# Kernel tuning notes

Hardware: AMD Instinct MI355X
Metric: run time of the kernel (lower is better)

The kernel has to match this reference:

```python
import jax, jax.numpy as jnp
import numpy as np

N_NODES = 50000
N_EDGES = 800000
F = 128
LN_EPS = 1e-5


def _sage_conv(h, src, dst, Wl, bl, Wr, n_nodes):
    # PyG SAGEConv (aggr='mean', root_weight=True):
    #   out_i = lin_l(mean_{j->i} h_j) + lin_r(h_i)
    msg = h[src]  # [E, F] irregular gather
    s = jax.ops.segment_sum(msg, dst, num_segments=n_nodes)  # [N, F]
    deg = jax.ops.segment_sum(jnp.ones((src.shape[0],), h.dtype), dst,
                              num_segments=n_nodes)  # [N]
    mean = s / jnp.maximum(deg, 1.0)[:, None]
    return mean @ Wl.T + bl + h @ Wr.T


def _graph_layernorm(h, w, b):
    # PyG LayerNorm mode='graph', batch=None: normalize over ALL entries,
    # eps added to std, then per-channel affine.
    m = h.mean()
    std = jnp.sqrt(jnp.mean((h - m) ** 2))
    return (h - m) / (std + LN_EPS) * w + b


def _prelu(h, w):
    # nn.PReLU(1): single shared slope
    return jnp.where(h >= 0, h, w * h)


def setup_inputs() -> dict:
    key = jax.random.key(0)
    ks = jax.random.split(key, 12)
    sc = 1.0 / np.sqrt(F)
    x = jax.random.normal(ks[0], (N_NODES, F), dtype=jnp.float32)
    edge_index = jax.random.randint(ks[1], (2, N_EDGES), 0, N_NODES, dtype=jnp.int64)
    return {
        "x": x,
        "edge_index": edge_index,
        "Wl0": jax.random.uniform(ks[2], (F, F), jnp.float32, -sc, sc),
        "bl0": jnp.zeros((F,), jnp.float32),
        "Wr0": jax.random.uniform(ks[3], (F, F), jnp.float32, -sc, sc),
        "ln_w0": jnp.ones((F,), jnp.float32),
        "ln_b0": jnp.zeros((F,), jnp.float32),
        "pw0": jnp.full((1,), 0.25, jnp.float32),
        "skipW0": jax.random.uniform(ks[4], (F, F), jnp.float32, -sc, sc),
        "Wl1": jax.random.uniform(ks[5], (F, F), jnp.float32, -sc, sc),
        "bl1": jnp.zeros((F,), jnp.float32),
        "Wr1": jax.random.uniform(ks[6], (F, F), jnp.float32, -sc, sc),
        "ln_w1": jnp.ones((F,), jnp.float32),
        "ln_b1": jnp.zeros((F,), jnp.float32),
        "pw1": jnp.full((1,), 0.25, jnp.float32),
    }


def reference(x, edge_index, Wl0, bl0, Wr0, ln_w0, ln_b0, pw0, skipW0,
              Wl1, bl1, Wr1, ln_w1, ln_b1, pw1):
    src, dst = edge_index[0], edge_index[1]
    n = x.shape[0]
    # layer 0: h = x
    h = _sage_conv(x, src, dst, Wl0, bl0, Wr0, n)
    h = _graph_layernorm(h, ln_w0, ln_b0)
    h1 = _prelu(h, pw0)
    # layer 1: h = skip(x) + h1
    h = x @ skipW0.T + h1
    h = _sage_conv(h, src, dst, Wl1, bl1, Wr1, n)
    h = _graph_layernorm(h, ln_w1, ln_b1)
    h = _prelu(h, pw1)
    return h
```

## Files before the change

kernel.cpp:

```cpp
#include <hip/hip_runtime.h>

#define LN_EPS 1e-5f
#define BUCKCAP 2048
#define PCHUNK 6656
#define PK 13

typedef short bf16x8 __attribute__((ext_vector_type(8)));
typedef float f32x4  __attribute__((ext_vector_type(4)));

static __device__ __forceinline__ float4 ld4(const float* p){ return *(const float4*)p; }
static __device__ __forceinline__ uint f2bf1(float f){
  uint u = __float_as_uint(f);
  return (u + 0x7fffu + ((u >> 16) & 1u)) >> 16;
}
static __device__ __forceinline__ float bf2f(uint lo16){ return __uint_as_float(lo16 << 16); }

__global__ void detect_fmt_kernel(const int* __restrict__ ei, int* __restrict__ flag,
                                  double* __restrict__ stats, int* __restrict__ bcnt){
  __shared__ int any;
  if (threadIdx.x == 0) any = 0;
  __syncthreads();
  int nz = 0;
  for (int i = threadIdx.x; i < 1024; i += 256)
    nz |= (ei[2*i+1] != 0);
  if (nz) atomicOr(&any, 1);
  for (int i = threadIdx.x; i < 1024; i += 256) bcnt[i] = 0;
  if (threadIdx.x < 4) stats[threadIdx.x] = 0.0;
  __syncthreads();
  if (threadIdx.x == 0) *flag = any;
}

__global__ __launch_bounds__(512) void partition_kernel(
    const int* __restrict__ ei, int E, const int* __restrict__ flag,
    int* __restrict__ bucket_count, uint* __restrict__ ebuf){
  __shared__ int hist[1024];
  __shared__ int base[1024];
  __shared__ int cur[1024];
  const int tid = threadIdx.x;
  const int lo = blockIdx.x * PCHUNK;
  const int hi = min(lo + PCHUNK, E);
  hist[tid] = 0; hist[tid + 512] = 0;
  __syncthreads();

  const int fmt = *flag;
  uint pd[PK];
  #pragma unroll
  for (int k = 0; k < PK; k++){
    int e = lo + tid + k*512;
    uint v = 0xffffffffu;
    if (e < hi){
      int s, d;
      if (fmt){ s = ei[e]; d = ei[E + e]; }
      else    { s = ei[2*e]; d = ei[2*(E + e)]; }
      v = ((uint)d << 16) | (uint)s;
      atomicAdd(&hist[v >> 22], 1);
    }
    pd[k] = v;
  }
  __syncthreads();
  #pragma unroll
  for (int t0 = 0; t0 < 2; t0++){
    int t = tid + t0*512;
    int h = hist[t];
    base[t] = (h > 0) ? atomicAdd(&bucket_count[t], h) : 0;
    cur[t] = 0;
  }
  __syncthreads();
  #pragma unroll
  for (int k = 0; k < PK; k++){
    int e = lo + tid + k*512;
    if (e < hi){
      uint v = pd[k];
      int b = v >> 22;
      int pos = base[b] + atomicAdd(&cur[b], 1);
      if (pos < BUCKCAP) ebuf[(size_t)b*BUCKCAP + pos] = v;
    }
  }
}

__global__ void convert_bf16_kernel(const float* __restrict__ src, ushort* __restrict__ dst, int n8){
  int i = blockIdx.x*256 + threadIdx.x;
  if (i >= n8) return;
  float4 a = ld4(src + (size_t)i*8);
  float4 b = ld4(src + (size_t)i*8 + 4);
  uint4 o;
  o.x = f2bf1(a.x) | (f2bf1(a.y) << 16);
  o.y = f2bf1(a.z) | (f2bf1(a.w) << 16);
  o.z = f2bf1(b.x) | (f2bf1(b.y) << 16);
  o.w = f2bf1(b.z) | (f2bf1(b.w) << 16);
  *(uint4*)(dst + (size_t)i*8) = o;
}

__global__ void convert_w_kernel(const float* __restrict__ s0, const float* __restrict__ s1,
                                 const float* __restrict__ s2, const float* __restrict__ s3,
                                 const float* __restrict__ s4, ushort* __restrict__ dst){
  int i = blockIdx.x*256 + threadIdx.x;
  if (i >= 10240) return;
  int m = i >> 11;
  int o = (i & 2047) * 8;
  const float* s = (m == 0) ? s0 : (m == 1) ? s1 : (m == 2) ? s2 : (m == 3) ? s3 : s4;
  float4 a = ld4(s + o);
  float4 b = ld4(s + o + 4);
  uint4 v;
  v.x = f2bf1(a.x) | (f2bf1(a.y) << 16);
  v.y = f2bf1(a.z) | (f2bf1(a.w) << 16);
  v.z = f2bf1(b.x) | (f2bf1(b.y) << 16);
  v.w = f2bf1(b.z) | (f2bf1(b.w) << 16);
  *(uint4*)(dst + (size_t)m*16384 + o) = v;
}

__global__ __launch_bounds__(512) void bucket_aggregate(const ushort* __restrict__ h,
    const uint* __restrict__ ebuf, const int* __restrict__ bucket_count,
    ushort* __restrict__ outmean, int N){
  __shared__ ushort ssrc[BUCKCAP];
  __shared__ int lcnt[64], lofs[64], lcur[64];
  const int tid = threadIdx.x;
  const int b = blockIdx.x;
  const int n0 = b << 6;
  const uint* eb = ebuf + (size_t)b*BUCKCAP;
  const int cnt = min(bucket_count[b], BUCKCAP);

  if (tid < 64) lcnt[tid] = 0;
  __syncthreads();
  for (int e = tid; e < cnt; e += 512)
    atomicAdd(&lcnt[(eb[e] >> 16) & 63], 1);
  __syncthreads();
  if (tid < 64){
    int v = lcnt[tid];
    int s = v;
    #pragma unroll
    for (int off = 1; off < 64; off <<= 1){
      int u = __shfl_up(s, off);
      if (tid >= off) s += u;
    }
    lofs[tid] = s - v;
    lcur[tid] = s - v;
  }
  __syncthreads();
  for (int e = tid; e < cnt; e += 512){
    uint v = eb[e];
    int pos = atomicAdd(&lcur[(v >> 16) & 63], 1);
    ssrc[pos] = (ushort)(v & 0xffffu);
  }
  __syncthreads();

  const int wv = tid >> 6, lane = tid & 63;
  const uint* hp = (const uint*)h;
  uint* op = (uint*)outmean;
  #pragma unroll 1
  for (int i = 0; i < 8; i++){
    int j = wv*8 + i;
    int node = n0 + j;
    if (node >= N) break;
    int start = lofs[j];
    int d = lcnt[j];
    float ax = 0.f, ay = 0.f;
    int e = 0;
    for (; e + 8 <= d; e += 8){
      uint v0 = hp[(size_t)ssrc[start+e+0]*64 + lane];
      uint v1 = hp[(size_t)ssrc[start+e+1]*64 + lane];
      uint v2 = hp[(size_t)ssrc[start+e+2]*64 + lane];
      uint v3 = hp[(size_t)ssrc[start+e+3]*64 + lane];
      uint v4 = hp[(size_t)ssrc[start+e+4]*64 + lane];
      uint v5 = hp[(size_t)ssrc[start+e+5]*64 + lane];
      uint v6 = hp[(size_t)ssrc[start+e+6]*64 + lane];
      uint v7 = hp[(size_t)ssrc[start+e+7]*64 + lane];
      ax += bf2f(v0 & 0xffffu) + bf2f(v1 & 0xffffu) + bf2f(v2 & 0xffffu) + bf2f(v3 & 0xffffu)
          + bf2f(v4 & 0xffffu) + bf2f(v5 & 0xffffu) + bf2f(v6 & 0xffffu) + bf2f(v7 & 0xffffu);
      ay += bf2f(v0 >> 16) + bf2f(v1 >> 16) + bf2f(v2 >> 16) + bf2f(v3 >> 16)
          + bf2f(v4 >> 16) + bf2f(v5 >> 16) + bf2f(v6 >> 16) + bf2f(v7 >> 16);
    }
    for (; e < d; e++){
      uint v = hp[(size_t)ssrc[start+e]*64 + lane];
      ax += bf2f(v & 0xffffu);
      ay += bf2f(v >> 16);
    }
    float inv = 1.f / fmaxf((float)d, 1.f);
    op[(size_t)node*64 + lane] = f2bf1(ax*inv) | (f2bf1(ay*inv) << 16);
  }
}

__global__ __launch_bounds__(256) void gemm_dual_mfma(
    const ushort* __restrict__ A1, const ushort* __restrict__ A2,
    const ushort* __restrict__ W1, const ushort* __restrict__ W2,
    const float* __restrict__ bias, float* __restrict__ out,
    int N, double* __restrict__ stats){
  const int tid  = threadIdx.x;
  const int lane = tid & 63;
  const int wv   = tid >> 6;
  const int r0   = blockIdx.x*128 + wv*32;
  const int lrow = lane & 15;
  const int lk   = (lane >> 4) * 8;

  f32x4 acc[2][8] = {};

  #pragma unroll
  for (int ks = 0; ks < 4; ks++){
    const int kb = ks*32 + lk;
    bf16x8 a1[2], a2[2];
    #pragma unroll
    for (int m = 0; m < 2; m++){
      int r = r0 + m*16 + lrow;
      if (r > N-1) r = N-1;
      a1[m] = *(const bf16x8*)(A1 + (size_t)r*128 + kb);
      a2[m] = *(const bf16x8*)(A2 + (size_t)r*128 + kb);
    }
    #pragma unroll
    for (int n = 0; n < 8; n++){
      const int c = n*16 + lrow;
      bf16x8 b1 = *(const bf16x8*)(W1 + c*128 + kb);
      bf16x8 b2 = *(const bf16x8*)(W2 + c*128 + kb);
      #pragma unroll
      for (int m = 0; m < 2; m++){
        acc[m][n] = __builtin_amdgcn_mfma_f32_16x16x32_bf16(a1[m], b1, acc[m][n], 0, 0, 0);
        acc[m][n] = __builtin_amdgcn_mfma_f32_16x16x32_bf16(a2[m], b2, acc[m][n], 0, 0, 0);
      }
    }
  }

  float bn[8];
  #pragma unroll
  for (int n = 0; n < 8; n++) bn[n] = bias[n*16 + lrow];

  double ls1 = 0.0, ls2 = 0.0;
  const int rb = (lane >> 4) * 4;
  #pragma unroll
  for (int m = 0; m < 2; m++){
    #pragma unroll
    for (int j = 0; j < 4; j++){
      int r = r0 + m*16 + rb + j;
      if (r < N){
        #pragma unroll
        for (int n = 0; n < 8; n++){
          float v = acc[m][n][j] + bn[n];
          out[(size_t)r*128 + n*16 + lrow] = v;
          ls1 += (double)v;
          ls2 += (double)v * (double)v;
        }
      }
    }
  }
  #pragma unroll
  for (int off = 32; off > 0; off >>= 1){
    ls1 += __shfl_down(ls1, off);
    ls2 += __shfl_down(ls2, off);
  }
  __shared__ double red[8];
  if (lane == 0){ red[wv*2] = ls1; red[wv*2+1] = ls2; }
  __syncthreads();
  if (tid == 0) atomicAdd(&stats[0], red[0]+red[2]+red[4]+red[6]);
  if (tid == 1) atomicAdd(&stats[1], red[1]+red[3]+red[5]+red[7]);
}

__global__ __launch_bounds__(256) void gemm_skip_mfma(
    const ushort* __restrict__ A, const ushort* __restrict__ W,
    const float* __restrict__ T0, const double* __restrict__ stats,
    const float* __restrict__ lnw, const float* __restrict__ lnb,
    const float* __restrict__ pw,
    ushort* __restrict__ outb, int N, double inv_cnt){
  const int tid  = threadIdx.x;
  const int lane = tid & 63;
  const int wv   = tid >> 6;
  const int r0   = blockIdx.x*128 + wv*32;
  const int lrow = lane & 15;
  const int lk   = (lane >> 4) * 8;

  f32x4 acc[2][8] = {};

  #pragma unroll
  for (int ks = 0; ks < 4; ks++){
    const int kb = ks*32 + lk;
    bf16x8 a[2];
    #pragma unroll
    for (int m = 0; m < 2; m++){
      int r = r0 + m*16 + lrow;
      if (r > N-1) r = N-1;
      a[m] = *(const bf16x8*)(A + (size_t)r*128 + kb);
    }
    #pragma unroll
    for (int n = 0; n < 8; n++){
      const int c = n*16 + lrow;
      bf16x8 b = *(const bf16x8*)(W + c*128 + kb);
      #pragma unroll
      for (int m = 0; m < 2; m++)
        acc[m][n] = __builtin_amdgcn_mfma_f32_16x16x32_bf16(a[m], b, acc[m][n], 0, 0, 0);
    }
  }

  double s1 = stats[0], s2 = stats[1];
  double md = s1 * inv_cnt;
  double var = s2 * inv_cnt - md*md;
  float mean = (float)md;
  float rstd = 1.f / ((float)sqrt(fmax(var, 0.0)) + LN_EPS);
  float slope = pw[0];
  float wn[8], bb[8];
  #pragma unroll
  for (int n = 0; n < 8; n++){
    wn[n] = lnw[n*16 + lrow];
    bb[n] = lnb[n*16 + lrow];
  }

  const int rb = (lane >> 4) * 4;
  #pragma unroll
  for (int m = 0; m < 2; m++){
    #pragma unroll
    for (int j = 0; j < 4; j++){
      int r = r0 + m*16 + rb + j;
      if (r < N){
        #pragma unroll
        for (int n = 0; n < 8; n++){
          float t = T0[(size_t)r*128 + n*16 + lrow];
          float l = (t - mean)*rstd*wn[n] + bb[n];
          l = (l >= 0.f) ? l : slope*l;
          float v = acc[m][n][j] + l;
          outb[(size_t)r*128 + n*16 + lrow] = (ushort)f2bf1(v);
        }
      }
    }
  }
}

__global__ __launch_bounds__(256) void ln_prelu_kernel(
    const float* __restrict__ T, const double* __restrict__ stats,
    const float* __restrict__ lnw, const float* __restrict__ lnb,
    const float* __restrict__ pw, float* __restrict__ out,
    int nf4, double inv_cnt){
  double s1 = stats[0], s2 = stats[1];
  double md = s1 * inv_cnt;
  double var = s2 * inv_cnt - md*md;
  float mean = (float)md;
  float rstd = 1.f / ((float)sqrt(fmax(var, 0.0)) + LN_EPS);
  float slope = pw[0];
  for (int i = blockIdx.x*256 + threadIdx.x; i < nf4; i += gridDim.x*256){
    int c4 = i & 31;
    float4 t = ld4(T + (size_t)i*4);
    float4 w4 = ld4(lnw + c4*4);
    float4 b4 = ld4(lnb + c4*4);
    float4 v; float l;
    l = (t.x - mean)*rstd*w4.x + b4.x; v.x = (l >= 0.f ? l : slope*l);
    l = (t.y - mean)*rstd*w4.y + b4.y; v.y = (l >= 0.f ? l : slope*l);
    l = (t.z - mean)*rstd*w4.z + b4.z; v.z = (l >= 0.f ? l : slope*l);
    l = (t.w - mean)*rstd*w4.w + b4.w; v.w = (l >= 0.f ? l : slope*l);
    *(float4*)(out + (size_t)i*4) = v;
  }
}

extern "C" void kernel_launch(void* const* d_in, const int* in_sizes, int n_in,
                              void* d_out, int out_size, void* d_ws, size_t ws_size,
                              hipStream_t stream){
  const float* x    = (const float*)d_in[0];
  const int*   ei   = (const int*)d_in[1];
  const float* Wl0  = (const float*)d_in[2];
  const float* bl0  = (const float*)d_in[3];
  const float* Wr0  = (const float*)d_in[4];
  const float* lnw0 = (const float*)d_in[5];
  const float* lnb0 = (const float*)d_in[6];
  const float* pw0  = (const float*)d_in[7];
  const float* skW  = (const float*)d_in[8];
  const float* Wl1  = (const float*)d_in[9];
  const float* bl1  = (const float*)d_in[10];
  const float* Wr1  = (const float*)d_in[11];
  const float* lnw1 = (const float*)d_in[12];
  const float* lnb1 = (const float*)d_in[13];
  const float* pw1  = (const float*)d_in[14];

  const int N = in_sizes[0] / 128;
  const int E = in_sizes[1] / 2;

  char* p = (char*)d_ws;
  auto carve = [&](size_t bytes)->char*{
    char* r = p;
    p += (bytes + 255) & ~(size_t)255;
    return r;
  };
  double* stats   = (double*)carve(4*sizeof(double));
  int*    flag    = (int*)carve(sizeof(int));
  int*    bcnt    = (int*)carve((size_t)1024*4);
  uint*   ebuf    = (uint*)carve((size_t)1024*BUCKCAP*4);
  ushort* x16     = (ushort*)carve((size_t)N*128*2);
  ushort* mean16  = (ushort*)carve((size_t)N*128*2);
  ushort* hskip16 = (ushort*)carve((size_t)N*128*2);
  ushort* wbuf    = (ushort*)carve((size_t)5*16384*2);
  float*  tbuf    = (float*)d_out;

  ushort* Wl0_16 = wbuf;
  ushort* Wr0_16 = wbuf + 16384;
  ushort* skW_16 = wbuf + 32768;
  ushort* Wl1_16 = wbuf + 49152;
  ushort* Wr1_16 = wbuf + 65536;

  const int nbuck = (N + 63) >> 6;
  const int pb = (E + PCHUNK - 1) / PCHUNK;
  detect_fmt_kernel<<<1, 256, 0, stream>>>(ei, flag, stats, bcnt);
  partition_kernel<<<pb, 512, 0, stream>>>(ei, E, flag, bcnt, ebuf);
  convert_bf16_kernel<<<(N*16 + 255)/256, 256, 0, stream>>>(x, x16, N*16);
  convert_w_kernel<<<40, 256, 0, stream>>>(Wl0, Wr0, skW, Wl1, Wr1, wbuf);

  int gb = (N + 127)/128;
  double inv_cnt = 1.0 / ((double)N * 128.0);

  bucket_aggregate<<<nbuck, 512, 0, stream>>>(x16, ebuf, bcnt, mean16, N);
  gemm_dual_mfma<<<gb, 256, 0, stream>>>(mean16, x16, Wl0_16, Wr0_16, bl0, tbuf, N, stats);
  gemm_skip_mfma<<<gb, 256, 0, stream>>>(x16, skW_16, tbuf, stats, lnw0, lnb0, pw0, hskip16, N, inv_cnt);
  bucket_aggregate<<<nbuck, 512, 0, stream>>>(hskip16, ebuf, bcnt, mean16, N);
  gemm_dual_mfma<<<gb, 256, 0, stream>>>(mean16, hskip16, Wl1_16, Wr1_16, bl1, tbuf, N, stats + 2);
  ln_prelu_kernel<<<2048, 256, 0, stream>>>(tbuf, stats + 2, lnw1, lnb1, pw1, (float*)d_out, N*32, inv_cnt);
}
```

Before: 269.6 us.

## Fuse GEMM, graph layernorm and PReLU via software grid barrier; merge prep kernels

Each layer's dual GEMM now keeps its accumulators in registers, reduces global stats, waits on an atomic-counter grid barrier, then applies layernorm, PReLU and (layer 0) the skip GEMM in place. This removes the fp32 intermediate round trip through global memory and the separate skip and layernorm kernels. Format detection moves into the partition kernel, and the x/weight conversions plus counter zeroing are merged into one prep kernel, cutting launches. The grid barrier needs all 391 blocks to be co-resident, which launch_bounds(256,2) is meant to allow; if they are not, it deadlocks.

Measured after the change: 312.0 us. 1.16x slower.

```diff
diff --git a/kernel.cpp b/kernel.cpp
--- a/kernel.cpp
+++ b/kernel.cpp
@@ -15,34 +15,63 @@
 }
 static __device__ __forceinline__ float bf2f(uint lo16){ return __uint_as_float(lo16 << 16); }
 
-__global__ void detect_fmt_kernel(const int* __restrict__ ei, int* __restrict__ flag,
-                                  double* __restrict__ stats, int* __restrict__ bcnt){
-  __shared__ int any;
-  if (threadIdx.x == 0) any = 0;
-  __syncthreads();
-  int nz = 0;
-  for (int i = threadIdx.x; i < 1024; i += 256)
-    nz |= (ei[2*i+1] != 0);
-  if (nz) atomicOr(&any, 1);
-  for (int i = threadIdx.x; i < 1024; i += 256) bcnt[i] = 0;
-  if (threadIdx.x < 4) stats[threadIdx.x] = 0.0;
-  __syncthreads();
-  if (threadIdx.x == 0) *flag = any;
+__global__ __launch_bounds__(256) void prep_kernel(
+    const float* __restrict__ x, ushort* __restrict__ x16, int nxb, int n8,
+    const float* __restrict__ s0, const float* __restrict__ s1,
+    const float* __restrict__ s2, const float* __restrict__ s3,
+    const float* __restrict__ s4, ushort* __restrict__ wdst,
+    double* __restrict__ stats, int* __restrict__ bcnt, int* __restrict__ cnts){
+  int bid = blockIdx.x, tid = threadIdx.x;
+  if (bid < nxb){
+    int i = bid*256 + tid;
+    if (i >= n8) return;
+    float4 a = ld4(x + (size_t)i*8);
+    float4 b = ld4(x + (size_t)i*8 + 4);
+    uint4 o;
+    o.x = f2bf1(a.x) | (f2bf1(a.y) << 16);
+    o.y = f2bf1(a.z) | (f2bf1(a.w) << 16);
+    o.z = f2bf1(b.x) | (f2bf1(b.y) << 16);
+    o.w = f2bf1(b.z) | (f2bf1(b.w) << 16);
+    *(uint4*)(x16 + (size_t)i*8) = o;
+  } else if (bid < nxb + 40){
+    int i = (bid - nxb)*256 + tid;
+    int m = i >> 11;
+    int o = (i & 2047) * 8;
+    const float* s = (m == 0) ? s0 : (m == 1) ? s1 : (m == 2) ? s2 : (m == 3) ? s3 : s4;
+    float4 a = ld4(s + o);
+    float4 b = ld4(s + o + 4);
+    uint4 v;
+    v.x = f2bf1(a.x) | (f2bf1(a.y) << 16);
+    v.y = f2bf1(a.z) | (f2bf1(a.w) << 16);
+    v.z = f2bf1(b.x) | (f2bf1(b.y) << 16);
+    v.w = f2bf1(b.z) | (f2bf1(b.w) << 16);
+    *(uint4*)(wdst + (size_t)m*16384 + o) = v;
+  } else {
+    bcnt[tid] = 0; bcnt[tid + 256] = 0; bcnt[tid + 512] = 0; bcnt[tid + 768] = 0;
+    if (tid < 4) stats[tid] = 0.0;
+    if (tid < 2) cnts[tid] = 0;
+  }
 }
 
 __global__ __launch_bounds__(512) void partition_kernel(
-    const int* __restrict__ ei, int E, const int* __restrict__ flag,
+    const int* __restrict__ ei, int E,
     int* __restrict__ bucket_count, uint* __restrict__ ebuf){
   __shared__ int hist[1024];
   __shared__ int base[1024];
   __shared__ int cur[1024];
+  __shared__ int anyv;
   const int tid = threadIdx.x;
   const int lo = blockIdx.x * PCHUNK;
   const int hi = min(lo + PCHUNK, E);
   hist[tid] = 0; hist[tid + 512] = 0;
-  __syncthreads();
-
-  const int fmt = *flag;
+  if (tid == 0) anyv = 0;
+  __syncthreads();
+  int nz = 0;
+  for (int i = tid; i < 1024; i += 512) nz |= (ei[2*i+1] != 0);
+  if (nz) atomicOr(&anyv, 1);
+  __syncthreads();
+  const int fmt = anyv;
+
   uint pd[PK];
   #pragma unroll
   for (int k = 0; k < PK; k++){
@@ -76,37 +105,6 @@
       if (pos < BUCKCAP) ebuf[(size_t)b*BUCKCAP + pos] = v;
     }
   }
-}
-
-__global__ void convert_bf16_kernel(const float* __restrict__ src, ushort* __restrict__ dst, int n8){
-  int i = blockIdx.x*256 + threadIdx.x;
-  if (i >= n8) return;
-  float4 a = ld4(src + (size_t)i*8);
-  float4 b = ld4(src + (size_t)i*8 + 4);
-  uint4 o;
-  o.x = f2bf1(a.x) | (f2bf1(a.y) << 16);
-  o.y = f2bf1(a.z) | (f2bf1(a.w) << 16);
-  o.z = f2bf1(b.x) | (f2bf1(b.y) << 16);
-  o.w = f2bf1(b.z) | (f2bf1(b.w) << 16);
-  *(uint4*)(dst + (size_t)i*8) = o;
-}
-
-__global__ void convert_w_kernel(const float* __restrict__ s0, const float* __restrict__ s1,
-                                 const float* __restrict__ s2, const float* __restrict__ s3,
-                                 const float* __restrict__ s4, ushort* __restrict__ dst){
-  int i = blockIdx.x*256 + threadIdx.x;
-  if (i >= 10240) return;
-  int m = i >> 11;
-  int o = (i & 2047) * 8;
-  const float* s = (m == 0) ? s0 : (m == 1) ? s1 : (m == 2) ? s2 : (m == 3) ? s3 : s4;
-  float4 a = ld4(s + o);
-  float4 b = ld4(s + o + 4);
-  uint4 v;
-  v.x = f2bf1(a.x) | (f2bf1(a.y) << 16);
-  v.y = f2bf1(a.z) | (f2bf1(a.w) << 16);
-  v.z = f2bf1(b.x) | (f2bf1(b.y) << 16);
-  v.w = f2bf1(b.z) | (f2bf1(b.w) << 16);
-  *(uint4*)(dst + (size_t)m*16384 + o) = v;
 }
 
 __global__ __launch_bounds__(512) void bucket_aggregate(const ushort* __restrict__ h,
@@ -180,11 +178,28 @@
   }
 }
 
-__global__ __launch_bounds__(256) void gemm_dual_mfma(
-    const ushort* __restrict__ A1, const ushort* __restrict__ A2,
-    const ushort* __restrict__ W1, const ushort* __restrict__ W2,
-    const float* __restrict__ bias, float* __restrict__ out,
-    int N, double* __restrict__ stats){
+static __device__ __forceinline__ void grid_barrier(int* cnt, int nblocks, int tid){
+  __syncthreads();
+  if (tid == 0){
+    __threadfence();
+    atomicAdd(cnt, 1);
+    while (__hip_atomic_load(cnt, __ATOMIC_ACQUIRE, __HIP_MEMORY_SCOPE_AGENT) < nblocks){
+      __builtin_amdgcn_s_sleep(8);
+    }
+    __threadfence();
+  }
+  __syncthreads();
+}
+
+__global__ __launch_bounds__(256, 2) void fused_layer0(
+    const ushort* __restrict__ A1 , const ushort* __restrict__ A2 ,
+    const ushort* __restrict__ Wl, const ushort* __restrict__ Wr,
+    const ushort* __restrict__ Wsk,
+    const float* __restrict__ bias,
+    const float* __restrict__ lnw, const float* __restrict__ lnb,
+    const float* __restrict__ pw,
+    ushort* __restrict__ outb, int N, double inv_cnt,
+    double* __restrict__ stats, int* __restrict__ bar){
   const int tid  = threadIdx.x;
   const int lane = tid & 63;
   const int wv   = tid >> 6;
@@ -192,7 +207,8 @@
   const int lrow = lane & 15;
   const int lk   = (lane >> 4) * 8;
 
-  f32x4 acc[2][8] = {};
+  f32x4 accD[2][8] = {};
+  f32x4 accS[2][8] = {};
 
   #pragma unroll
   for (int ks = 0; ks < 4; ks++){
@@ -208,19 +224,25 @@
     #pragma unroll
     for (int n = 0; n < 8; n++){
       const int c = n*16 + lrow;
-      bf16x8 b1 = *(const bf16x8*)(W1 + c*128 + kb);
-      bf16x8 b2 = *(const bf16x8*)(W2 + c*128 + kb);
+      bf16x8 bl = *(const bf16x8*)(Wl  + c*128 + kb);
+      bf16x8 br = *(const bf16x8*)(Wr  + c*128 + kb);
+      bf16x8 bs = *(const bf16x8*)(Wsk + c*128 + kb);
       #pragma unroll
       for (int m = 0; m < 2; m++){
-        acc[m][n] = __builtin_amdgcn_mfma_f32_16x16x32_bf16(a1[m], b1, acc[m][n], 0, 0, 0);
-        acc[m][n] = __builtin_amdgcn_mfma_f32_16x16x32_bf16(a2[m], b2, acc[m][n], 0, 0, 0);
-      }
-    }
-  }
-
-  float bn[8];
-  #pragma unroll
-  for (int n = 0; n < 8; n++) bn[n] = bias[n*16 + lrow];
+        accD[m][n] = __builtin_amdgcn_mfma_f32_16x16x32_bf16(a1[m], bl, accD[m][n], 0, 0, 0);
+        accD[m][n] = __builtin_amdgcn_mfma_f32_16x16x32_bf16(a2[m], br, accD[m][n], 0, 0, 0);
+        accS[m][n] = __builtin_amdgcn_mfma_f32_16x16x32_bf16(a2[m], bs, accS[m][n], 0, 0, 0);
+      }
+    }
+  }
+
+  float bn[8], wn[8], bb[8];
+  #pragma unroll
+  for (int n = 0; n < 8; n++){
+    bn[n] = bias[n*16 + lrow];
+    wn[n] = lnw[n*16 + lrow];
+    bb[n] = lnb[n*16 + lrow];
+  }
 
   double ls1 = 0.0, ls2 = 0.0;
   const int rb = (lane >> 4) * 4;
@@ -232,8 +254,7 @@
       if (r < N){
         #pragma unroll
         for (int n = 0; n < 8; n++){
-          float v = acc[m][n][j] + bn[n];
-          out[(size_t)r*128 + n*16 + lrow] = v;
+          float v = accD[m][n][j] + bn[n];
           ls1 += (double)v;
           ls2 += (double)v * (double)v;
         }
@@ -248,16 +269,48 @@
   __shared__ double red[8];
   if (lane == 0){ red[wv*2] = ls1; red[wv*2+1] = ls2; }
   __syncthreads();
-  if (tid == 0) atomicAdd(&stats[0], red[0]+red[2]+red[4]+red[6]);
-  if (tid == 1) atomicAdd(&stats[1], red[1]+red[3]+red[5]+red[7]);
-}
-
-__global__ __launch_bounds__(256) void gemm_skip_mfma(
-    const ushort* __restrict__ A, const ushort* __restrict__ W,
-    const float* __restrict__ T0, const double* __restrict__ stats,
+  if (tid == 0){
+    atomicAdd(&stats[0], red[0]+red[2]+red[4]+red[6]);
+    atomicAdd(&stats[1], red[1]+red[3]+red[5]+red[7]);
+  }
+
+  grid_barrier(bar, gridDim.x, tid);
+
+  double s1 = __hip_atomic_load(&stats[0], __ATOMIC_RELAXED, __HIP_MEMORY_SCOPE_AGENT);
+  double s2 = __hip_atomic_load(&stats[1], __ATOMIC_RELAXED, __HIP_MEMORY_SCOPE_AGENT);
+  double md = s1 * inv_cnt;
+  double var = s2 * inv_cnt - md*md;
+  float mean = (float)md;
+  float rstd = 1.f / ((float)sqrt(fmax(var, 0.0)) + LN_EPS);
+  float slope = pw[0];
+
+  #pragma unroll
+  for (int m = 0; m < 2; m++){
+    #pragma unroll
+    for (int j = 0; j < 4; j++){
+      int r = r0 + m*16 + rb + j;
+      if (r < N){
+        #pragma unroll
+        for (int n = 0; n < 8; n++){
+          float t = accD[m][n][j] + bn[n];
+          float l = (t - mean)*rstd*wn[n] + bb[n];
+          l = (l >= 0.f) ? l : slope*l;
+          float v = accS[m][n][j] + l;
+          outb[(size_t)r*128 + n*16 + lrow] = (ushort)f2bf1(v);
+        }
+      }
+    }
+  }
+}
+
+__global__ __launch_bounds__(256, 2) void fused_layer1(
+    const ushort* __restrict__ A1 , const ushort* __restrict__ A2 ,
+    const ushort* __restrict__ Wl, const ushort* __restrict__ Wr,
+    const float* __restrict__ bias,
     const float* __restrict__ lnw, const float* __restrict__ lnb,
     const float* __restrict__ pw,
-    ushort* __restrict__ outb, int N, double inv_cnt){
+    float* __restrict__ out, int N, double inv_cnt,
+    double* __restrict__ stats, int* __restrict__ bar){
   const int tid  = threadIdx.x;
   const int lane = tid & 63;
   const int wv   = tid >> 6;
@@ -265,42 +318,80 @@
   const int lrow = lane & 15;
   const int lk   = (lane >> 4) * 8;
 
-  f32x4 acc[2][8] = {};
+  f32x4 accD[2][8] = {};
 
   #pragma unroll
   for (int ks = 0; ks < 4; ks++){
     const int kb = ks*32 + lk;
-    bf16x8 a[2];
+    bf16x8 a1[2], a2[2];
     #pragma unroll
     for (int m = 0; m < 2; m++){
       int r = r0 + m*16 + lrow;
       if (r > N-1) r = N-1;
-      a[m] = *(const bf16x8*)(A + (size_t)r*128 + kb);
+      a1[m] = *(const bf16x8*)(A1 + (size_t)r*128 + kb);
+      a2[m] = *(const bf16x8*)(A2 + (size_t)r*128 + kb);
     }
     #pragma unroll
     for (int n = 0; n < 8; n++){
       const int c = n*16 + lrow;
-      bf16x8 b = *(const bf16x8*)(W + c*128 + kb);
+      bf16x8 bl = *(const bf16x8*)(Wl + c*128 + kb);
+      bf16x8 br = *(const bf16x8*)(Wr + c*128 + kb);
       #pragma unroll
-      for (int m = 0; m < 2; m++)
-        acc[m][n] = __builtin_amdgcn_mfma_f32_16x16x32_bf16(a[m], b, acc[m][n], 0, 0, 0);
-    }
-  }
-
-  double s1 = stats[0], s2 = stats[1];
+      for (int m = 0; m < 2; m++){
+        accD[m][n] = __builtin_amdgcn_mfma_f32_16x16x32_bf16(a1[m], bl, accD[m][n], 0, 0, 0);
+        accD[m][n] = __builtin_amdgcn_mfma_f32_16x16x32_bf16(a2[m], br, accD[m][n], 0, 0, 0);
+      }
+    }
+  }
+
+  float bn[8], wn[8], bb[8];
+  #pragma unroll
+  for (int n = 0; n < 8; n++){
+    bn[n] = bias[n*16 + lrow];
+    wn[n] = lnw[n*16 + lrow];
+    bb[n] = lnb[n*16 + lrow];
+  }
+
+  double ls1 = 0.0, ls2 = 0.0;
+  const int rb = (lane >> 4) * 4;
+  #pragma unroll
+  for (int m = 0; m < 2; m++){
+    #pragma unroll
+    for (int j = 0; j < 4; j++){
+      int r = r0 + m*16 + rb + j;
+      if (r < N){
+        #pragma unroll
+        for (int n = 0; n < 8; n++){
+          float v = accD[m][n][j] + bn[n];
+          ls1 += (double)v;
+          ls2 += (double)v * (double)v;
+        }
+      }
+    }
+  }
+  #pragma unroll
+  for (int off = 32; off > 0; off >>= 1){
+    ls1 += __shfl_down(ls1, off);
+    ls2 += __shfl_down(ls2, off);
+  }
+  __shared__ double red[8];
+  if (lane == 0){ red[wv*2] = ls1; red[wv*2+1] = ls2; }
+  __syncthreads();
+  if (tid == 0){
+    atomicAdd(&stats[0], red[0]+red[2]+red[4]+red[6]);
+    atomicAdd(&stats[1], red[1]+red[3]+red[5]+red[7]);
+  }
+
+  grid_barrier(bar, gridDim.x, tid);
+
+  double s1 = __hip_atomic_load(&stats[0], __ATOMIC_RELAXED, __HIP_MEMORY_SCOPE_AGENT);
+  double s2 = __hip_atomic_load(&stats[1], __ATOMIC_RELAXED, __HIP_MEMORY_SCOPE_AGENT);
   double md = s1 * inv_cnt;
   double var = s2 * inv_cnt - md*md;
   float mean = (float)md;
   float rstd = 1.f / ((float)sqrt(fmax(var, 0.0)) + LN_EPS);
   float slope = pw[0];
-  float wn[8], bb[8];
-  #pragma unroll
-  for (int n = 0; n < 8; n++){
-    wn[n] = lnw[n*16 + lrow];
-    bb[n] = lnb[n*16 + lrow];
-  }
-
-  const int rb = (lane >> 4) * 4;
+
   #pragma unroll
   for (int m = 0; m < 2; m++){
     #pragma unroll
@@ -309,39 +400,13 @@
       if (r < N){
         #pragma unroll
         for (int n = 0; n < 8; n++){
-          float t = T0[(size_t)r*128 + n*16 + lrow];
+          float t = accD[m][n][j] + bn[n];
           float l = (t - mean)*rstd*wn[n] + bb[n];
           l = (l >= 0.f) ? l : slope*l;
-          float v = acc[m][n][j] + l;
-          outb[(size_t)r*128 + n*16 + lrow] = (ushort)f2bf1(v);
+          out[(size_t)r*128 + n*16 + lrow] = l;
         }
       }
     }
-  }
-}
-
-__global__ __launch_bounds__(256) void ln_prelu_kernel(
-    const float* __restrict__ T, const double* __restrict__ stats,
-    const float* __restrict__ lnw, const float* __restrict__ lnb,
-    const float* __restrict__ pw, float* __restrict__ out,
-    int nf4, double inv_cnt){
-  double s1 = stats[0], s2 = stats[1];
-  double md = s1 * inv_cnt;
-  double var = s2 * inv_cnt - md*md;
-  float mean = (float)md;
-  float rstd = 1.f / ((float)sqrt(fmax(var, 0.0)) + LN_EPS);
-  float slope = pw[0];
-  for (int i = blockIdx.x*256 + threadIdx.x; i < nf4; i += gridDim.x*256){
-    int c4 = i & 31;
-    float4 t = ld4(T + (size_t)i*4);
-    float4 w4 = ld4(lnw + c4*4);
-    float4 b4 = ld4(lnb + c4*4);
-    float4 v; float l;
-    l = (t.x - mean)*rstd*w4.x + b4.x; v.x = (l >= 0.f ? l : slope*l);
-    l = (t.y - mean)*rstd*w4.y + b4.y; v.y = (l >= 0.f ? l : slope*l);
-    l = (t.z - mean)*rstd*w4.z + b4.z; v.z = (l >= 0.f ? l : slope*l);
-    l = (t.w - mean)*rstd*w4.w + b4.w; v.w = (l >= 0.f ? l : slope*l);
-    *(float4*)(out + (size_t)i*4) = v;
   }
 }
 
@@ -374,14 +439,13 @@
     return r;
   };
   double* stats   = (double*)carve(4*sizeof(double));
-  int*    flag    = (int*)carve(sizeof(int));
+  int*    cnts    = (int*)carve(2*sizeof(int));
   int*    bcnt    = (int*)carve((size_t)1024*4);
   uint*   ebuf    = (uint*)carve((size_t)1024*BUCKCAP*4);
   ushort* x16     = (ushort*)carve((size_t)N*128*2);
   ushort* mean16  = (ushort*)carve((size_t)N*128*2);
   ushort* hskip16 = (ushort*)carve((size_t)N*128*2);
   ushort* wbuf    = (ushort*)carve((size_t)5*16384*2);
-  float*  tbuf    = (float*)d_out;
 
   ushort* Wl0_16 = wbuf;
   ushort* Wr0_16 = wbuf + 16384;
@@ -389,20 +453,21 @@
   ushort* Wl1_16 = wbuf + 49152;
   ushort* Wr1_16 = wbuf + 65536;
 
+  const int n8  = N*16;
+  const int nxb = (n8 + 255)/256;
   const int nbuck = (N + 63) >> 6;
   const int pb = (E + PCHUNK - 1) / PCHUNK;
-  detect_fmt_kernel<<<1, 256, 0, stream>>>(ei, flag, stats, bcnt);
-  partition_kernel<<<pb, 512, 0, stream>>>(ei, E, flag, bcnt, ebuf);
-  convert_bf16_kernel<<<(N*16 + 255)/256, 256, 0, stream>>>(x, x16, N*16);
-  convert_w_kernel<<<40, 256, 0, stream>>>(Wl0, Wr0, skW, Wl1, Wr1, wbuf);
-
-  int gb = (N + 127)/128;
-  double inv_cnt = 1.0 / ((double)N * 128.0);
+  const int gb = (N + 127)/128;
+  const double inv_cnt = 1.0 / ((double)N * 128.0);
+
+  prep_kernel<<<nxb + 40 + 1, 256, 0, stream>>>(x, x16, nxb, n8,
+      Wl0, Wr0, skW, Wl1, Wr1, wbuf, stats, bcnt, cnts);
+  partition_kernel<<<pb, 512, 0, stream>>>(ei, E, bcnt, ebuf);
 
   bucket_aggregate<<<nbuck, 512, 0, stream>>>(x16, ebuf, bcnt, mean16, N);
-  gemm_dual_mfma<<<gb, 256, 0, stream>>>(mean16, x16, Wl0_16, Wr0_16, bl0, tbuf, N, stats);
-  gemm_skip_mfma<<<gb, 256, 0, stream>>>(x16, skW_16, tbuf, stats, lnw0, lnb0, pw0, hskip16, N, inv_cnt);
+  fused_layer0<<<gb, 256, 0, stream>>>(mean16, x16, Wl0_16, Wr0_16, skW_16,
+      bl0, lnw0, lnb0, pw0, hskip16, N, inv_cnt, stats, &cnts[0]);
   bucket_aggregate<<<nbuck, 512, 0, stream>>>(hskip16, ebuf, bcnt, mean16, N);
-  gemm_dual_mfma<<<gb, 256, 0, stream>>>(mean16, hskip16, Wl1_16, Wr1_16, bl1, tbuf, N, stats + 2);
-  ln_prelu_kernel<<<2048, 256, 0, stream>>>(tbuf, stats + 2, lnw1, lnb1, pw1, (float*)d_out, N*32, inv_cnt);
-}
+  fused_layer1<<<gb, 256, 0, stream>>>(mean16, hskip16, Wl1_16, Wr1_16,
+      bl1, lnw1, lnb1, pw1, (float*)d_out, N, inv_cnt, stats + 2, &cnts[1]);
+}
```
